# Performance work log

Hardware: AMD Instinct MI355X
Metric: run time of the kernel (lower is better)

Reference implementation:

```python
import jax, jax.numpy as jnp
import numpy as np

N = 100000   # nodes
E = 1600000  # edges (avg degree 16)
D = 128      # embedding / hidden dim
L = 2        # aggregator layers (len(weight_size_list)-1)
EPS = 1e-12  # F.normalize eps


def setup_inputs() -> dict:
    key = jax.random.key(0)
    ks = jax.random.split(key, 8)
    return {
        "embeddings": jax.random.normal(ks[0], (N, D), jnp.float32),
        "edge_src": jax.random.randint(ks[1], (E,), 0, N, jnp.int32),
        "edge_dst": jax.random.randint(ks[2], (E,), 0, N, jnp.int32),
        "edge_val": jax.random.uniform(ks[3], (E,), jnp.float32),
        "W_sum": jax.random.normal(ks[4], (L, D, D), jnp.float32) * 0.05,
        "b_sum": jnp.zeros((L, D), jnp.float32),
        "W_prod": jax.random.normal(ks[5], (L, D, D), jnp.float32) * 0.05,
        "b_prod": jnp.zeros((L, D), jnp.float32),
    }


def reference(embeddings, edge_src, edge_dst, edge_val, W_sum, b_sum, W_prod, b_prod):
    # Faithful KGATConv forward with BiAggregator (alg_type='bi'), dropout=0 (eval).
    # Note: original code feeds the UN-normalized aggregator output as `embeddings`
    # (ego) to the next layer, while the SpMM consumes the normalized all_embeddings[-1].
    ego = embeddings            # `embeddings` variable in torch code
    spmm_in = embeddings        # all_embeddings[-1]
    outs = [embeddings]
    for i in range(L):
        # sparse A @ x : gather source rows, scale by edge value, scatter-add to dst
        msg = edge_val[:, None] * spmm_in[edge_src]            # [E, D]
        side = jax.ops.segment_sum(msg, edge_dst, num_segments=N)  # [N, D]
        # BiAggregator: LeakyReLU(W1(e+side)+b1) + LeakyReLU(W2(e*side)+b2)
        s = jax.nn.leaky_relu((ego + side) @ W_sum[i] + b_sum[i], 0.01)
        p = jax.nn.leaky_relu((ego * side) @ W_prod[i] + b_prod[i], 0.01)
        ego = s + p
        # F.normalize(p=2, dim=-1)
        nrm = jnp.maximum(jnp.linalg.norm(ego, axis=-1, keepdims=True), EPS)
        spmm_in = ego / nrm
        outs.append(spmm_in)
    return jnp.stack(outs)  # [L+1, N, D]
```

## Files before the change

### kernel.cpp

```cpp
#include <hip/hip_runtime.h>

#define D_DIM 128
#define ROWS 32
#define MROWS 64
#define ZPAD 136
#define EPAD 132

#define BSH 7
#define BROWS (1 << BSH)
#define NB_MAX 2048
#define CHUNK 4096

typedef __bf16 bf16x8 __attribute__((ext_vector_type(8)));
typedef __bf16 bf16x4 __attribute__((ext_vector_type(4)));
typedef float  f32x4  __attribute__((ext_vector_type(4)));

__global__ __launch_bounds__(256) void spmm_atomic(
    const float* __restrict__ x, const int* __restrict__ src,
    const int* __restrict__ dst, const float* __restrict__ val,
    float* __restrict__ side, long long total)
{
    long long i = (long long)blockIdx.x * blockDim.x + threadIdx.x;
    if (i >= total) return;
    int e = (int)(i >> 5);
    int q = (int)(i & 31);
    int s = src[e];
    int d = dst[e];
    float v = val[e];
    const float4 xv = *reinterpret_cast<const float4*>(x + (long long)s * D_DIM + q * 4);
    float* o = side + (long long)d * D_DIM + q * 4;
    unsafeAtomicAdd(o + 0, v * xv.x);
    unsafeAtomicAdd(o + 1, v * xv.y);
    unsafeAtomicAdd(o + 2, v * xv.z);
    unsafeAtomicAdd(o + 3, v * xv.w);
}

__global__ __launch_bounds__(256) void hist_kernel(
    const int* __restrict__ dst, int* __restrict__ cnt, int E)
{
    int i = blockIdx.x * 256 + threadIdx.x;
    if (i < E) atomicAdd(&cnt[dst[i]], 1);
}

__global__ __launch_bounds__(256) void scan_blocks(
    const int* __restrict__ cnt, int* __restrict__ row_ptr,
    int* __restrict__ blk_sums, int N)
{
    __shared__ int sh[256];
    int i = blockIdx.x * 256 + threadIdx.x;
    int v = (i < N) ? cnt[i] : 0;
    sh[threadIdx.x] = v;
    __syncthreads();
#pragma unroll
    for (int off = 1; off < 256; off <<= 1) {
        int t = (threadIdx.x >= off) ? sh[threadIdx.x - off] : 0;
        __syncthreads();
        sh[threadIdx.x] += t;
        __syncthreads();
    }
    if (i < N) row_ptr[i] = sh[threadIdx.x] - v;
    if (threadIdx.x == 255) blk_sums[blockIdx.x] = sh[255];
}

__global__ __launch_bounds__(256) void scan_carry(int* __restrict__ blk, int B)
{
    __shared__ int sh[256];
    __shared__ int carry;
    if (threadIdx.x == 0) carry = 0;
    __syncthreads();
    for (int base = 0; base < B; base += 256) {
        int i = base + threadIdx.x;
        int v = (i < B) ? blk[i] : 0;
        sh[threadIdx.x] = v;
        __syncthreads();
#pragma unroll
        for (int off = 1; off < 256; off <<= 1) {
            int t = (threadIdx.x >= off) ? sh[threadIdx.x - off] : 0;
            __syncthreads();
            sh[threadIdx.x] += t;
            __syncthreads();
        }
        int excl = sh[threadIdx.x] - v + carry;
        if (i < B) blk[i] = excl;
        __syncthreads();
        if (threadIdx.x == 255) carry = carry + sh[255];
        __syncthreads();
    }
}

__global__ __launch_bounds__(256) void scan_add(
    int* __restrict__ row_ptr, const int* __restrict__ blk_sums,
    int* __restrict__ row_fill, int N, int E)
{
    int i = blockIdx.x * 256 + threadIdx.x;
    if (i < N) {
        int v = row_ptr[i] + blk_sums[i >> 8];
        row_ptr[i]  = v;
        row_fill[i] = v;
    }
    if (i == 0) row_ptr[N] = E;
}

__global__ __launch_bounds__(256) void scatter_kernel(
    const int* __restrict__ src, const int* __restrict__ dst,
    const float* __restrict__ val, int* __restrict__ row_fill,
    int2* __restrict__ csr_sv, int E)
{
    int e = blockIdx.x * 256 + threadIdx.x;
    if (e >= E) return;
    int d = dst[e];
    int pos = atomicAdd(&row_fill[d], 1);
    csr_sv[pos] = make_int2(src[e], __float_as_int(val[e]));
}

__global__ __launch_bounds__(256) void bucket_count(
    const int* __restrict__ dst, int* __restrict__ bucket_cnt, int E, int NB)
{
    __shared__ int h[NB_MAX];
    for (int i = threadIdx.x; i < NB; i += 256) h[i] = 0;
    __syncthreads();
    int ebase = blockIdx.x * CHUNK;
    int ecnt  = min(CHUNK, E - ebase);
    for (int i = threadIdx.x; i < ecnt; i += 256)
        atomicAdd(&h[dst[ebase + i] >> BSH], 1);
    __syncthreads();
    for (int i = threadIdx.x; i < NB; i += 256)
        if (h[i]) atomicAdd(&bucket_cnt[i], h[i]);
}

__global__ __launch_bounds__(256) void bucket_scan(
    const int* __restrict__ bucket_cnt, int* __restrict__ bucket_ptr,
    int* __restrict__ bucket_fill, int NB, int E)
{
    __shared__ int sh[256];
    __shared__ int carry;
    if (threadIdx.x == 0) carry = 0;
    __syncthreads();
    for (int base = 0; base < NB; base += 256) {
        int i = base + threadIdx.x;
        int v = (i < NB) ? bucket_cnt[i] : 0;
        sh[threadIdx.x] = v;
        __syncthreads();
#pragma unroll
        for (int off = 1; off < 256; off <<= 1) {
            int t = (threadIdx.x >= off) ? sh[threadIdx.x - off] : 0;
            __syncthreads();
            sh[threadIdx.x] += t;
            __syncthreads();
        }
        if (i < NB) {
            int excl = sh[threadIdx.x] - v + carry;
            bucket_ptr[i]  = excl;
            bucket_fill[i] = excl;
        }
        __syncthreads();
        if (threadIdx.x == 255) carry = carry + sh[255];
        __syncthreads();
    }
    if (threadIdx.x == 0) bucket_ptr[NB] = E;
}

__global__ __launch_bounds__(256) void bucket_scatter(
    const int* __restrict__ src, const int* __restrict__ dst,
    const float* __restrict__ val, int* __restrict__ bucket_fill,
    int* __restrict__ stage,
    int NB, int E)
{
    __shared__ int hist[NB_MAX];
    __shared__ int excl[NB_MAX];
    __shared__ int gbase[NB_MAX];
    __shared__ int psum[256];
    __shared__ int s_src[CHUNK];
    __shared__ int s_val[CHUNK];
    __shared__ int s_dst[CHUNK];

    const int tid   = threadIdx.x;
    const int ebase = blockIdx.x * CHUNK;
    const int ecnt  = min(CHUNK, E - ebase);

    for (int i = tid; i < NB; i += 256) hist[i] = 0;
    __syncthreads();
    for (int i = tid; i < ecnt; i += 256)
        atomicAdd(&hist[dst[ebase + i] >> BSH], 1);
    __syncthreads();
    const int per = (NB + 255) / 256;
    const int t0  = tid * per;
    int tsum = 0;
    for (int k = 0; k < per; ++k) {
        int idx = t0 + k;
        tsum += (idx < NB) ? hist[idx] : 0;
    }
    psum[tid] = tsum;
    __syncthreads();
#pragma unroll
    for (int off = 1; off < 256; off <<= 1) {
        int t = (tid >= off) ? psum[tid - off] : 0;
        __syncthreads();
        psum[tid] += t;
        __syncthreads();
    }
    int run = psum[tid] - tsum;
    for (int k = 0; k < per; ++k) {
        int idx = t0 + k;
        if (idx < NB) { excl[idx] = run; run += hist[idx]; }
    }
    __syncthreads();
    for (int i = tid; i < NB; i += 256)
        gbase[i] = hist[i] ? atomicAdd(&bucket_fill[i], hist[i]) : 0;
    __syncthreads();
    for (int i = tid; i < NB; i += 256) hist[i] = excl[i];
    __syncthreads();
    for (int i = tid; i < ecnt; i += 256) {
        int d = dst[ebase + i];
        int slot = atomicAdd(&hist[d >> BSH], 1);
        s_src[slot] = src[ebase + i];
        s_val[slot] = __float_as_int(val[ebase + i]);
        s_dst[slot] = d;
    }
    __syncthreads();
    for (int i = tid; i < ecnt; i += 256) {
        int d   = s_dst[i];
        int bkt = d >> BSH;
        int gpos = gbase[bkt] + (i - excl[bkt]);
        *reinterpret_cast<int4*>(stage + 4 * (long long)gpos) =
            make_int4(s_src[i], s_val[i], d, 0);
    }
}

__global__ __launch_bounds__(256) void bucket_finalize(
    const int* __restrict__ stage, const int* __restrict__ bucket_ptr,
    int* __restrict__ row_ptr, int2* __restrict__ csr_sv, int N, int E)
{
    __shared__ int cnt[BROWS];
    __shared__ int rbase[BROWS];

    const int b   = blockIdx.x;
    const int tid = threadIdx.x;
    const int e0  = bucket_ptr[b];
    const int e1  = bucket_ptr[b + 1];
    const int r0  = b << BSH;
    const int nrows = min(BROWS, N - r0);

    if (tid < BROWS) cnt[tid] = 0;
    __syncthreads();
    for (int i = e0 + tid; i < e1; i += 256)
        atomicAdd(&cnt[stage[4 * (long long)i + 2] & (BROWS - 1)], 1);
    __syncthreads();
    if (tid < BROWS) rbase[tid] = cnt[tid];
    __syncthreads();
#pragma unroll
    for (int off = 1; off < BROWS; off <<= 1) {
        int t = 0;
        if (tid < BROWS && tid >= off) t = rbase[tid - off];
        __syncthreads();
        if (tid < BROWS) rbase[tid] += t;
        __syncthreads();
    }
    if (tid < BROWS) {
        int excl = e0 + rbase[tid] - cnt[tid];
        rbase[tid] = excl;
        if (tid < nrows) row_ptr[r0 + tid] = excl;
    }
    if (b == 0 && tid == 0) row_ptr[N] = E;
    __syncthreads();
    if (tid < BROWS) cnt[tid] = 0;
    __syncthreads();
    for (int i = e0 + tid; i < e1; i += 256) {
        const int4 t = *reinterpret_cast<const int4*>(stage + 4 * (long long)i);
        int r = t.z & (BROWS - 1);
        int rank = atomicAdd(&cnt[r], 1);
        csr_sv[rbase[r] + rank] = make_int2(t.x, t.y);
    }
}

__global__ __launch_bounds__(256) void wt_convert(
    const float* __restrict__ Wsum, const float* __restrict__ Wprod,
    __bf16* __restrict__ WTsum, __bf16* __restrict__ WTprod, int total)
{
    int i = blockIdx.x * 256 + threadIdx.x;
    if (i >= total) return;
    int l  = i >> 14;
    int nk = i & 16383;
    int n  = nk >> 7;
    int k  = nk & 127;
    int widx = (l << 14) + (k << 7) + n;
    WTsum[i]  = (__bf16)Wsum[widx];
    WTprod[i] = (__bf16)Wprod[widx];
}

__global__ __launch_bounds__(256) void emb_prep(
    const float* __restrict__ emb, float* __restrict__ out0,
    __bf16* __restrict__ xbf, long long n4)
{
    long long i = (long long)blockIdx.x * 256 + threadIdx.x;
    if (i >= n4) return;
    float4 v = reinterpret_cast<const float4*>(emb)[i];
    reinterpret_cast<float4*>(out0)[i] = v;
    bf16x4 b;
    b[0] = (__bf16)v.x; b[1] = (__bf16)v.y;
    b[2] = (__bf16)v.z; b[3] = (__bf16)v.w;
    reinterpret_cast<bf16x4*>(xbf)[i] = b;
}

__global__ __launch_bounds__(256) void spmm_csr_bf16(
    const __bf16* __restrict__ x, const int* __restrict__ row_ptr,
    const int2* __restrict__ csr_sv, float* __restrict__ side, int N)
{
    int row  = blockIdx.x * 8 + (threadIdx.x >> 5);
    int lane = threadIdx.x & 31;
    if (row >= N) return;
    int start = row_ptr[row];
    int end   = row_ptr[row + 1];
    const __bf16* xl = x + lane * 4;
    float4 acc = make_float4(0.f, 0.f, 0.f, 0.f);
    int j = start;
    for (; j + 8 <= end; j += 8) {
        int2 sv0 = csr_sv[j + 0], sv1 = csr_sv[j + 1];
        int2 sv2 = csr_sv[j + 2], sv3 = csr_sv[j + 3];
        int2 sv4 = csr_sv[j + 4], sv5 = csr_sv[j + 5];
        int2 sv6 = csr_sv[j + 6], sv7 = csr_sv[j + 7];
        bf16x4 b0 = *reinterpret_cast<const bf16x4*>(xl + (long long)sv0.x * D_DIM);
        bf16x4 b1 = *reinterpret_cast<const bf16x4*>(xl + (long long)sv1.x * D_DIM);
        bf16x4 b2 = *reinterpret_cast<const bf16x4*>(xl + (long long)sv2.x * D_DIM);
        bf16x4 b3 = *reinterpret_cast<const bf16x4*>(xl + (long long)sv3.x * D_DIM);
        bf16x4 b4 = *reinterpret_cast<const bf16x4*>(xl + (long long)sv4.x * D_DIM);
        bf16x4 b5 = *reinterpret_cast<const bf16x4*>(xl + (long long)sv5.x * D_DIM);
        bf16x4 b6 = *reinterpret_cast<const bf16x4*>(xl + (long long)sv6.x * D_DIM);
        bf16x4 b7 = *reinterpret_cast<const bf16x4*>(xl + (long long)sv7.x * D_DIM);
        float v0 = __int_as_float(sv0.y), v1 = __int_as_float(sv1.y);
        float v2 = __int_as_float(sv2.y), v3 = __int_as_float(sv3.y);
        float v4 = __int_as_float(sv4.y), v5 = __int_as_float(sv5.y);
        float v6 = __int_as_float(sv6.y), v7 = __int_as_float(sv7.y);
        acc.x += v0 * (float)b0[0] + v1 * (float)b1[0] + v2 * (float)b2[0] + v3 * (float)b3[0];
        acc.y += v0 * (float)b0[1] + v1 * (float)b1[1] + v2 * (float)b2[1] + v3 * (float)b3[1];
        acc.z += v0 * (float)b0[2] + v1 * (float)b1[2] + v2 * (float)b2[2] + v3 * (float)b3[2];
        acc.w += v0 * (float)b0[3] + v1 * (float)b1[3] + v2 * (float)b2[3] + v3 * (float)b3[3];
        acc.x += v4 * (float)b4[0] + v5 * (float)b5[0] + v6 * (float)b6[0] + v7 * (float)b7[0];
        acc.y += v4 * (float)b4[1] + v5 * (float)b5[1] + v6 * (float)b6[1] + v7 * (float)b7[1];
        acc.z += v4 * (float)b4[2] + v5 * (float)b5[2] + v6 * (float)b6[2] + v7 * (float)b7[2];
        acc.w += v4 * (float)b4[3] + v5 * (float)b5[3] + v6 * (float)b6[3] + v7 * (float)b7[3];
    }
    for (; j + 4 <= end; j += 4) {
        int2 sv0 = csr_sv[j + 0], sv1 = csr_sv[j + 1];
        int2 sv2 = csr_sv[j + 2], sv3 = csr_sv[j + 3];
        bf16x4 b0 = *reinterpret_cast<const bf16x4*>(xl + (long long)sv0.x * D_DIM);
        bf16x4 b1 = *reinterpret_cast<const bf16x4*>(xl + (long long)sv1.x * D_DIM);
        bf16x4 b2 = *reinterpret_cast<const bf16x4*>(xl + (long long)sv2.x * D_DIM);
        bf16x4 b3 = *reinterpret_cast<const bf16x4*>(xl + (long long)sv3.x * D_DIM);
        float v0 = __int_as_float(sv0.y), v1 = __int_as_float(sv1.y);
        float v2 = __int_as_float(sv2.y), v3 = __int_as_float(sv3.y);
        acc.x += v0 * (float)b0[0] + v1 * (float)b1[0] + v2 * (float)b2[0] + v3 * (float)b3[0];
        acc.y += v0 * (float)b0[1] + v1 * (float)b1[1] + v2 * (float)b2[1] + v3 * (float)b3[1];
        acc.z += v0 * (float)b0[2] + v1 * (float)b1[2] + v2 * (float)b2[2] + v3 * (float)b3[2];
        acc.w += v0 * (float)b0[3] + v1 * (float)b1[3] + v2 * (float)b2[3] + v3 * (float)b3[3];
    }
    for (; j < end; ++j) {
        int2 sv = csr_sv[j];
        float v = __int_as_float(sv.y);
        bf16x4 b = *reinterpret_cast<const bf16x4*>(xl + (long long)sv.x * D_DIM);
        acc.x += v * (float)b[0];
        acc.y += v * (float)b[1];
        acc.z += v * (float)b[2];
        acc.w += v * (float)b[3];
    }
    *reinterpret_cast<float4*>(side + (long long)row * D_DIM + lane * 4) = acc;
}

__global__ __launch_bounds__(256) void spmm_csr_f32(
    const float* __restrict__ x, const int* __restrict__ row_ptr,
    const int2* __restrict__ csr_sv, float* __restrict__ side, int N)
{
    int row  = blockIdx.x * 8 + (threadIdx.x >> 5);
    int lane = threadIdx.x & 31;
    if (row >= N) return;
    int start = row_ptr[row];
    int end   = row_ptr[row + 1];
    const float* xl = x + lane * 4;
    float4 acc = make_float4(0.f, 0.f, 0.f, 0.f);
    int j = start;
    for (; j + 4 <= end; j += 4) {
        int2 sv0 = csr_sv[j + 0], sv1 = csr_sv[j + 1];
        int2 sv2 = csr_sv[j + 2], sv3 = csr_sv[j + 3];
        const float4 x0 = *reinterpret_cast<const float4*>(xl + (long long)sv0.x * D_DIM);
        const float4 x1 = *reinterpret_cast<const float4*>(xl + (long long)sv1.x * D_DIM);
        const float4 x2 = *reinterpret_cast<const float4*>(xl + (long long)sv2.x * D_DIM);
        const float4 x3 = *reinterpret_cast<const float4*>(xl + (long long)sv3.x * D_DIM);
        float v0 = __int_as_float(sv0.y), v1 = __int_as_float(sv1.y);
        float v2 = __int_as_float(sv2.y), v3 = __int_as_float(sv3.y);
        acc.x += v0 * x0.x + v1 * x1.x + v2 * x2.x + v3 * x3.x;
        acc.y += v0 * x0.y + v1 * x1.y + v2 * x2.y + v3 * x3.y;
        acc.z += v0 * x0.z + v1 * x1.z + v2 * x2.z + v3 * x3.z;
        acc.w += v0 * x0.w + v1 * x1.w + v2 * x2.w + v3 * x3.w;
    }
    for (; j < end; ++j) {
        int2 sv = csr_sv[j];
        float v = __int_as_float(sv.y);
        const float4 xv = *reinterpret_cast<const float4*>(xl + (long long)sv.x * D_DIM);
        acc.x += v * xv.x;
        acc.y += v * xv.y;
        acc.z += v * xv.z;
        acc.w += v * xv.w;
    }
    *reinterpret_cast<float4*>(side + (long long)row * D_DIM + lane * 4) = acc;
}

__global__ __launch_bounds__(512) void fused_layer_mfma(
    const float* __restrict__ ego_src, const float* __restrict__ nrm_in,
    const float* __restrict__ side,
    const __bf16* __restrict__ WTsum, const float* __restrict__ bsum,
    const __bf16* __restrict__ WTprod, const float* __restrict__ bprod,
    float* __restrict__ norm_out,
    __bf16* __restrict__ nbf_out,
    float* __restrict__ nrm_out,
    int N)
{
    __shared__ __align__(16) char smem[MROWS * ZPAD * 2 * sizeof(__bf16)];
    __shared__ float rowsq[MROWS][9];
    auto zt = reinterpret_cast<__bf16(*)[ZPAD]>(smem);
    auto mt = reinterpret_cast<__bf16(*)[ZPAD]>(smem + MROWS * ZPAD * sizeof(__bf16));
    auto et = reinterpret_cast<float(*)[EPAD]>(smem);

    const int tid  = threadIdx.x;
    const int row0 = blockIdx.x * MROWS;

    for (int idx = tid; idx < MROWS * 32; idx += 512) {
        int r = idx >> 5, q = idx & 31;
        int row = row0 + r;
        float4 e4 = make_float4(0.f, 0.f, 0.f, 0.f);
        float4 s4 = make_float4(0.f, 0.f, 0.f, 0.f);
        if (row < N) {
            e4 = *reinterpret_cast<const float4*>(ego_src + (long long)row * D_DIM + q * 4);
            s4 = *reinterpret_cast<const float4*>(side    + (long long)row * D_DIM + q * 4);
            if (nrm_in) {
                float sc = nrm_in[row];
                e4.x *= sc; e4.y *= sc; e4.z *= sc; e4.w *= sc;
            }
        }
        bf16x4 z4, m4;
        z4[0] = (__bf16)(e4.x + s4.x); z4[1] = (__bf16)(e4.y + s4.y);
        z4[2] = (__bf16)(e4.z + s4.z); z4[3] = (__bf16)(e4.w + s4.w);
        m4[0] = (__bf16)(e4.x * s4.x); m4[1] = (__bf16)(e4.y * s4.y);
        m4[2] = (__bf16)(e4.z * s4.z); m4[3] = (__bf16)(e4.w * s4.w);
        *reinterpret_cast<bf16x4*>(&zt[r][q * 4]) = z4;
        *reinterpret_cast<bf16x4*>(&mt[r][q * 4]) = m4;
    }

    const int wave = tid >> 6;
    const int lane = tid & 63;
    const int ln   = lane & 15;
    const int quad = lane >> 4;

    bf16x8 bs[4], bp[4];
#pragma unroll
    for (int ks = 0; ks < 4; ++ks) {
        const long long wofs = (long long)(wave * 16 + ln) * D_DIM + ks * 32 + quad * 8;
        bs[ks] = *reinterpret_cast<const bf16x8*>(WTsum  + wofs);
        bp[ks] = *reinterpret_cast<const bf16x8*>(WTprod + wofs);
    }

    __syncthreads();

    f32x4 acc_s[4], acc_p[4];
#pragma unroll
    for (int rg = 0; rg < 4; ++rg) {
        acc_s[rg] = (f32x4){0.f, 0.f, 0.f, 0.f};
        acc_p[rg] = (f32x4){0.f, 0.f, 0.f, 0.f};
    }

#pragma unroll
    for (int rg = 0; rg < 4; ++rg) {
#pragma unroll
        for (int ks = 0; ks < 4; ++ks) {
            const int k0 = ks * 32 + quad * 8;
            bf16x8 az = *reinterpret_cast<const bf16x8*>(&zt[rg * 16 + ln][k0]);
            bf16x8 am = *reinterpret_cast<const bf16x8*>(&mt[rg * 16 + ln][k0]);
            acc_s[rg] = __builtin_amdgcn_mfma_f32_16x16x32_bf16(az, bs[ks], acc_s[rg], 0, 0, 0);
            acc_p[rg] = __builtin_amdgcn_mfma_f32_16x16x32_bf16(am, bp[ks], acc_p[rg], 0, 0, 0);
        }
    }

    const float bsv = bsum[wave * 16 + ln];
    const float bpv = bprod[wave * 16 + ln];
#pragma unroll
    for (int rg = 0; rg < 4; ++rg) {
#pragma unroll
        for (int r = 0; r < 4; ++r) {
            float sv = acc_s[rg][r] + bsv;
            sv = sv > 0.f ? sv : 0.01f * sv;
            float pv = acc_p[rg][r] + bpv;
            pv = pv > 0.f ? pv : 0.01f * pv;
            float e = sv + pv;
            acc_s[rg][r] = e;
            float sq = e * e;
#pragma unroll
            for (int off = 1; off < 16; off <<= 1)
                sq += __shfl_xor(sq, off, 16);
            if (ln == 0)
                rowsq[rg * 16 + quad * 4 + r][wave] = sq;
        }
    }

    __syncthreads();

#pragma unroll
    for (int rg = 0; rg < 4; ++rg)
#pragma unroll
        for (int r = 0; r < 4; ++r)
            et[rg * 16 + quad * 4 + r][wave * 16 + ln] = acc_s[rg][r];
    __syncthreads();

    for (int idx = tid; idx < MROWS * 32; idx += 512) {
        int r = idx >> 5, q = idx & 31;
        int row = row0 + r;
        if (row >= N) continue;
        float s = 0.f;
#pragma unroll
        for (int j = 0; j < 8; ++j) s += rowsq[r][j];
        float nrmv = fmaxf(sqrtf(s), 1e-12f);
        float inv  = 1.0f / nrmv;
        if (q == 0 && nrm_out) nrm_out[row] = nrmv;
        float4 e4 = *reinterpret_cast<const float4*>(&et[r][q * 4]);
        float4 n4 = make_float4(e4.x * inv, e4.y * inv, e4.z * inv, e4.w * inv);
        *reinterpret_cast<float4*>(norm_out + (long long)row * D_DIM + q * 4) = n4;
        if (nbf_out) {
            bf16x4 b4;
            b4[0] = (__bf16)n4.x; b4[1] = (__bf16)n4.y;
            b4[2] = (__bf16)n4.z; b4[3] = (__bf16)n4.w;
            *reinterpret_cast<bf16x4*>(nbf_out + (long long)row * D_DIM + q * 4) = b4;
        }
    }
}

__global__ __launch_bounds__(256) void fused_layer_f32(
    const float* __restrict__ ego, const float* __restrict__ side,
    const float* __restrict__ Wsum, const float* __restrict__ bsum,
    const float* __restrict__ Wprod, const float* __restrict__ bprod,
    float* __restrict__ ego_out, float* __restrict__ norm_out, int N)
{
    __shared__ float zt[ROWS][D_DIM];
    __shared__ float mt[ROWS][D_DIM];
    __shared__ float wsh[32][D_DIM];
    __shared__ float wph[32][D_DIM];

    const int tid  = threadIdx.x;
    const int row0 = blockIdx.x * ROWS;
    const int cg   = tid & 31;
    const int rg   = tid >> 5;

    for (int idx = tid; idx < ROWS * 32; idx += 256) {
        int r = idx >> 5, q = idx & 31;
        int row = row0 + r;
        float4 e4 = make_float4(0.f, 0.f, 0.f, 0.f);
        float4 s4 = make_float4(0.f, 0.f, 0.f, 0.f);
        if (row < N) {
            e4 = *reinterpret_cast<const float4*>(ego  + (long long)row * D_DIM + q * 4);
            s4 = *reinterpret_cast<const float4*>(side + (long long)row * D_DIM + q * 4);
        }
        float4 z4 = make_float4(e4.x + s4.x, e4.y + s4.y, e4.z + s4.z, e4.w + s4.w);
        float4 m4 = make_float4(e4.x * s4.x, e4.y * s4.y, e4.z * s4.z, e4.w * s4.w);
        *reinterpret_cast<float4*>(&zt[r][q * 4]) = z4;
        *reinterpret_cast<float4*>(&mt[r][q * 4]) = m4;
    }

    float acc_s[4][4], acc_p[4][4];
#pragma unroll
    for (int a = 0; a < 4; ++a)
#pragma unroll
        for (int b = 0; b < 4; ++b) { acc_s[a][b] = 0.f; acc_p[a][b] = 0.f; }

    for (int kc = 0; kc < D_DIM; kc += 32) {
        __syncthreads();
        for (int idx = tid; idx < 32 * 32; idx += 256) {
            int kk = idx >> 5, q = idx & 31;
            *reinterpret_cast<float4*>(&wsh[kk][q * 4]) =
                *reinterpret_cast<const float4*>(Wsum + (long long)(kc + kk) * D_DIM + q * 4);
            *reinterpret_cast<float4*>(&wph[kk][q * 4]) =
                *reinterpret_cast<const float4*>(Wprod + (long long)(kc + kk) * D_DIM + q * 4);
        }
        __syncthreads();
#pragma unroll 8
        for (int kk = 0; kk < 32; ++kk) {
            float4 w_s = *reinterpret_cast<const float4*>(&wsh[kk][cg * 4]);
            float4 w_p = *reinterpret_cast<const float4*>(&wph[kk][cg * 4]);
#pragma unroll
            for (int rr = 0; rr < 4; ++rr) {
                float z = zt[rg * 4 + rr][kc + kk];
                float m = mt[rg * 4 + rr][kc + kk];
                acc_s[rr][0] += z * w_s.x; acc_s[rr][1] += z * w_s.y;
                acc_s[rr][2] += z * w_s.z; acc_s[rr][3] += z * w_s.w;
                acc_p[rr][0] += m * w_p.x; acc_p[rr][1] += m * w_p.y;
                acc_p[rr][2] += m * w_p.z; acc_p[rr][3] += m * w_p.w;
            }
        }
    }

    const float4 bs = *reinterpret_cast<const float4*>(bsum  + cg * 4);
    const float4 bp = *reinterpret_cast<const float4*>(bprod + cg * 4);
    float ev[4][4];
    float part[4];
#pragma unroll
    for (int rr = 0; rr < 4; ++rr) {
        float bsv[4] = {bs.x, bs.y, bs.z, bs.w};
        float bpv[4] = {bp.x, bp.y, bp.z, bp.w};
        float acc = 0.f;
#pragma unroll
        for (int cc = 0; cc < 4; ++cc) {
            float sv = acc_s[rr][cc] + bsv[cc];
            sv = sv > 0.f ? sv : 0.01f * sv;
            float pv = acc_p[rr][cc] + bpv[cc];
            pv = pv > 0.f ? pv : 0.01f * pv;
            float e = sv + pv;
            ev[rr][cc] = e;
            acc += e * e;
        }
        part[rr] = acc;
    }
#pragma unroll
    for (int off = 1; off < 32; off <<= 1) {
#pragma unroll
        for (int rr = 0; rr < 4; ++rr)
            part[rr] += __shfl_xor(part[rr], off, 32);
    }
#pragma unroll
    for (int rr = 0; rr < 4; ++rr) {
        int row = row0 + rg * 4 + rr;
        if (row >= N) continue;
        float inv = 1.0f / fmaxf(sqrtf(part[rr]), 1e-12f);
        float4 o  = make_float4(ev[rr][0] * inv, ev[rr][1] * inv,
                                ev[rr][2] * inv, ev[rr][3] * inv);
        *reinterpret_cast<float4*>(norm_out + (long long)row * D_DIM + cg * 4) = o;
        if (ego_out) {
            float4 g = make_float4(ev[rr][0], ev[rr][1], ev[rr][2], ev[rr][3]);
            *reinterpret_cast<float4*>(ego_out + (long long)row * D_DIM + cg * 4) = g;
        }
    }
}

extern "C" void kernel_launch(void* const* d_in, const int* in_sizes, int n_in,
                              void* d_out, int out_size, void* d_ws, size_t ws_size,
                              hipStream_t stream)
{
    const float* emb   = (const float*)d_in[0];
    const int*   esrc  = (const int*)  d_in[1];
    const int*   edst  = (const int*)  d_in[2];
    const float* evalv = (const float*)d_in[3];
    const float* Wsum  = (const float*)d_in[4];
    const float* bsum  = (const float*)d_in[5];
    const float* Wprod = (const float*)d_in[6];
    const float* bprod = (const float*)d_in[7];
    float* out = (float*)d_out;

    const int D = 128;
    const int N = in_sizes[0] / D;
    const int E = in_sizes[1];
    const int L = in_sizes[5] / D;
    const size_t ND = (size_t)N * D;
    const int B = (N + 255) / 256;
    const int NB = (N + BROWS - 1) >> BSH;

    char* ws = (char*)d_ws;
    float* side    = (float*)ws;                 ws += ND * sizeof(float);
    float* ego_buf = (float*)ws;                 ws += ND * sizeof(float);
    int*   row_ptr  = (int*)ws;                  ws += (size_t)(N + 1) * sizeof(int);
    int*   row_fill = (int*)ws;                  ws += (size_t)N * sizeof(int);
    int*   blk_sums = (int*)ws;                  ws += (size_t)B * sizeof(int);
    ws = (char*)(((uintptr_t)ws + 15) & ~(uintptr_t)15);
    int2*  csr_sv   = (int2*)ws;                 ws += (size_t)E * sizeof(int2);
    size_t csr_bytes = (size_t)(ws - (char*)d_ws);
    __bf16* WTsum  = (__bf16*)ws;                ws += (size_t)L * D * D * sizeof(__bf16);
    __bf16* WTprod = (__bf16*)ws;                ws += (size_t)L * D * D * sizeof(__bf16);
    __bf16* xbf    = (__bf16*)ws;                ws += ND * sizeof(__bf16);
    float*  nrm_buf = (float*)ws;                ws += (size_t)N * sizeof(float);
    size_t mfma_bytes = (size_t)(ws - (char*)d_ws);
    int* bucket_cnt  = (int*)ws;                 ws += (size_t)(NB + 1) * sizeof(int);
    int* bucket_ptr  = (int*)ws;                 ws += (size_t)(NB + 1) * sizeof(int);
    int* bucket_fill = (int*)ws;                 ws += (size_t)(NB + 1) * sizeof(int);
    size_t bucket_bytes = (size_t)(ws - (char*)d_ws);
    int* stage = (int*)side;

    const bool use_csr    = (ws_size >= csr_bytes);
    const bool use_mfma   = (ws_size >= mfma_bytes);
    const bool use_bucket = use_csr && (ws_size >= bucket_bytes) && (NB <= NB_MAX) &&
                            ((size_t)E * 16 <= 2 * ND * sizeof(float));

    if (use_mfma) {
        long long n4 = (long long)(ND / 4);
        emb_prep<<<(int)((n4 + 255) / 256), 256, 0, stream>>>(emb, out, xbf, n4);
        int total = L * D * D;
        wt_convert<<<(total + 255) / 256, 256, 0, stream>>>(
            Wsum, Wprod, WTsum, WTprod, total);
    } else {
        hipMemcpyAsync(out, emb, ND * sizeof(float), hipMemcpyDeviceToDevice, stream);
    }

    if (use_bucket) {
        const int nblk = (E + CHUNK - 1) / CHUNK;
        hipMemsetAsync(bucket_cnt, 0, (size_t)NB * sizeof(int), stream);
        bucket_count<<<nblk, 256, 0, stream>>>(edst, bucket_cnt, E, NB);
        bucket_scan<<<1, 256, 0, stream>>>(bucket_cnt, bucket_ptr, bucket_fill, NB, E);
        bucket_scatter<<<nblk, 256, 0, stream>>>(
            esrc, edst, evalv, bucket_fill, stage, NB, E);
        bucket_finalize<<<NB, 256, 0, stream>>>(
            stage, bucket_ptr, row_ptr, csr_sv, N, E);
    } else if (use_csr) {
        hipMemsetAsync(row_fill, 0, (size_t)N * sizeof(int), stream);
        hist_kernel<<<(E + 255) / 256, 256, 0, stream>>>(edst, row_fill, E);
        scan_blocks<<<B, 256, 0, stream>>>(row_fill, row_ptr, blk_sums, N);
        scan_carry<<<1, 256, 0, stream>>>(blk_sums, B);
        scan_add<<<B, 256, 0, stream>>>(row_ptr, blk_sums, row_fill, N, E);
        scatter_kernel<<<(E + 255) / 256, 256, 0, stream>>>(
            esrc, edst, evalv, row_fill, csr_sv, E);
    }

    const float* ego      = emb;
    const float* nrm_prev = nullptr;
    const float* spmm_in  = emb;
    for (int l = 0; l < L; ++l) {
        if (use_csr) {
            if (use_mfma) {
                spmm_csr_bf16<<<(N + 7) / 8, 256, 0, stream>>>(
                    xbf, row_ptr, csr_sv, side, N);
            } else {
                spmm_csr_f32<<<(N + 7) / 8, 256, 0, stream>>>(
                    spmm_in, row_ptr, csr_sv, side, N);
            }
        } else {
            hipMemsetAsync(side, 0, ND * sizeof(float), stream);
            long long total  = (long long)E * 32;
            long long blocks = (total + 255) / 256;
            spmm_atomic<<<(int)blocks, 256, 0, stream>>>(spmm_in, esrc, edst, evalv,
                                                         side, total);
        }

        float* norm_out = out + (size_t)(l + 1) * ND;
        if (use_mfma) {
            const bool more = (l + 1 < L);
            __bf16* nbf  = more ? xbf : nullptr;
            float*  nrmo = more ? nrm_buf : nullptr;
            fused_layer_mfma<<<(N + MROWS - 1) / MROWS, 512, 0, stream>>>(
                ego, nrm_prev, side,
                WTsum + (size_t)l * D * D, bsum + (size_t)l * D,
                WTprod + (size_t)l * D * D, bprod + (size_t)l * D,
                norm_out, nbf, nrmo, N);
            ego      = norm_out;
            nrm_prev = nrm_buf;
        } else {
            float* ego_out = (l + 1 < L) ? ego_buf : nullptr;
            fused_layer_f32<<<(N + ROWS - 1) / ROWS, 256, 0, stream>>>(
                ego, side,
                Wsum + (size_t)l * D * D, bsum + (size_t)l * D,
                Wprod + (size_t)l * D * D, bprod + (size_t)l * D,
                ego_out, norm_out, N);
            ego     = ego_buf;
            spmm_in = norm_out;
        }
    }
}
```

Before: 535.0 us.

## Fuse CSR SpMM gather into the MFMA layer kernel and ping-pong bf16 buffers

```diff
diff --git a/kernel.cpp b/kernel.cpp
--- a/kernel.cpp
+++ b/kernel.cpp
@@ -300,70 +300,6 @@
     b[0] = (__bf16)v.x; b[1] = (__bf16)v.y;
     b[2] = (__bf16)v.z; b[3] = (__bf16)v.w;
     reinterpret_cast<bf16x4*>(xbf)[i] = b;
-}
-
-__global__ __launch_bounds__(256) void spmm_csr_bf16(
-    const __bf16* __restrict__ x, const int* __restrict__ row_ptr,
-    const int2* __restrict__ csr_sv, float* __restrict__ side, int N)
-{
-    int row  = blockIdx.x * 8 + (threadIdx.x >> 5);
-    int lane = threadIdx.x & 31;
-    if (row >= N) return;
-    int start = row_ptr[row];
-    int end   = row_ptr[row + 1];
-    const __bf16* xl = x + lane * 4;
-    float4 acc = make_float4(0.f, 0.f, 0.f, 0.f);
-    int j = start;
-    for (; j + 8 <= end; j += 8) {
-        int2 sv0 = csr_sv[j + 0], sv1 = csr_sv[j + 1];
-        int2 sv2 = csr_sv[j + 2], sv3 = csr_sv[j + 3];
-        int2 sv4 = csr_sv[j + 4], sv5 = csr_sv[j + 5];
-        int2 sv6 = csr_sv[j + 6], sv7 = csr_sv[j + 7];
-        bf16x4 b0 = *reinterpret_cast<const bf16x4*>(xl + (long long)sv0.x * D_DIM);
-        bf16x4 b1 = *reinterpret_cast<const bf16x4*>(xl + (long long)sv1.x * D_DIM);
-        bf16x4 b2 = *reinterpret_cast<const bf16x4*>(xl + (long long)sv2.x * D_DIM);
-        bf16x4 b3 = *reinterpret_cast<const bf16x4*>(xl + (long long)sv3.x * D_DIM);
-        bf16x4 b4 = *reinterpret_cast<const bf16x4*>(xl + (long long)sv4.x * D_DIM);
-        bf16x4 b5 = *reinterpret_cast<const bf16x4*>(xl + (long long)sv5.x * D_DIM);
-        bf16x4 b6 = *reinterpret_cast<const bf16x4*>(xl + (long long)sv6.x * D_DIM);
-        bf16x4 b7 = *reinterpret_cast<const bf16x4*>(xl + (long long)sv7.x * D_DIM);
-        float v0 = __int_as_float(sv0.y), v1 = __int_as_float(sv1.y);
-        float v2 = __int_as_float(sv2.y), v3 = __int_as_float(sv3.y);
-        float v4 = __int_as_float(sv4.y), v5 = __int_as_float(sv5.y);
-        float v6 = __int_as_float(sv6.y), v7 = __int_as_float(sv7.y);
-        acc.x += v0 * (float)b0[0] + v1 * (float)b1[0] + v2 * (float)b2[0] + v3 * (float)b3[0];
-        acc.y += v0 * (float)b0[1] + v1 * (float)b1[1] + v2 * (float)b2[1] + v3 * (float)b3[1];
-        acc.z += v0 * (float)b0[2] + v1 * (float)b1[2] + v2 * (float)b2[2] + v3 * (float)b3[2];
-        acc.w += v0 * (float)b0[3] + v1 * (float)b1[3] + v2 * (float)b2[3] + v3 * (float)b3[3];
-        acc.x += v4 * (float)b4[0] + v5 * (float)b5[0] + v6 * (float)b6[0] + v7 * (float)b7[0];
-        acc.y += v4 * (float)b4[1] + v5 * (float)b5[1] + v6 * (float)b6[1] + v7 * (float)b7[1];
-        acc.z += v4 * (float)b4[2] + v5 * (float)b5[2] + v6 * (float)b6[2] + v7 * (float)b7[2];
-        acc.w += v4 * (float)b4[3] + v5 * (float)b5[3] + v6 * (float)b6[3] + v7 * (float)b7[3];
-    }
-    for (; j + 4 <= end; j += 4) {
-        int2 sv0 = csr_sv[j + 0], sv1 = csr_sv[j + 1];
-        int2 sv2 = csr_sv[j + 2], sv3 = csr_sv[j + 3];
-        bf16x4 b0 = *reinterpret_cast<const bf16x4*>(xl + (long long)sv0.x * D_DIM);
-        bf16x4 b1 = *reinterpret_cast<const bf16x4*>(xl + (long long)sv1.x * D_DIM);
-        bf16x4 b2 = *reinterpret_cast<const bf16x4*>(xl + (long long)sv2.x * D_DIM);
-        bf16x4 b3 = *reinterpret_cast<const bf16x4*>(xl + (long long)sv3.x * D_DIM);
-        float v0 = __int_as_float(sv0.y), v1 = __int_as_float(sv1.y);
-        float v2 = __int_as_float(sv2.y), v3 = __int_as_float(sv3.y);
-        acc.x += v0 * (float)b0[0] + v1 * (float)b1[0] + v2 * (float)b2[0] + v3 * (float)b3[0];
-        acc.y += v0 * (float)b0[1] + v1 * (float)b1[1] + v2 * (float)b2[1] + v3 * (float)b3[1];
-        acc.z += v0 * (float)b0[2] + v1 * (float)b1[2] + v2 * (float)b2[2] + v3 * (float)b3[2];
-        acc.w += v0 * (float)b0[3] + v1 * (float)b1[3] + v2 * (float)b2[3] + v3 * (float)b3[3];
-    }
-    for (; j < end; ++j) {
-        int2 sv = csr_sv[j];
-        float v = __int_as_float(sv.y);
-        bf16x4 b = *reinterpret_cast<const bf16x4*>(xl + (long long)sv.x * D_DIM);
-        acc.x += v * (float)b[0];
-        acc.y += v * (float)b[1];
-        acc.z += v * (float)b[2];
-        acc.w += v * (float)b[3];
-    }
-    *reinterpret_cast<float4*>(side + (long long)row * D_DIM + lane * 4) = acc;
 }
 
 __global__ __launch_bounds__(256) void spmm_csr_f32(
@@ -405,8 +341,9 @@
 }
 
 __global__ __launch_bounds__(512) void fused_layer_mfma(
+    const __bf16* __restrict__ xbf, const int* __restrict__ row_ptr,
+    const int2* __restrict__ csr_sv,
     const float* __restrict__ ego_src, const float* __restrict__ nrm_in,
-    const float* __restrict__ side,
     const __bf16* __restrict__ WTsum, const float* __restrict__ bsum,
     const __bf16* __restrict__ WTprod, const float* __restrict__ bprod,
     float* __restrict__ norm_out,
@@ -423,26 +360,80 @@
     const int tid  = threadIdx.x;
     const int row0 = blockIdx.x * MROWS;
 
-    for (int idx = tid; idx < MROWS * 32; idx += 512) {
-        int r = idx >> 5, q = idx & 31;
-        int row = row0 + r;
-        float4 e4 = make_float4(0.f, 0.f, 0.f, 0.f);
-        float4 s4 = make_float4(0.f, 0.f, 0.f, 0.f);
+    const int grp = tid >> 5;
+    const int gl  = tid & 31;
+    const __bf16* xl = xbf + gl * 4;
+
+    for (int rr = 0; rr < 4; ++rr) {
+        const int r   = grp * 4 + rr;
+        const int row = row0 + r;
+        float4 acc = make_float4(0.f, 0.f, 0.f, 0.f);
+        float4 e4  = make_float4(0.f, 0.f, 0.f, 0.f);
         if (row < N) {
-            e4 = *reinterpret_cast<const float4*>(ego_src + (long long)row * D_DIM + q * 4);
-            s4 = *reinterpret_cast<const float4*>(side    + (long long)row * D_DIM + q * 4);
+            int j   = row_ptr[row];
+            int end = row_ptr[row + 1];
+            for (; j + 8 <= end; j += 8) {
+                int2 sv0 = csr_sv[j + 0], sv1 = csr_sv[j + 1];
+                int2 sv2 = csr_sv[j + 2], sv3 = csr_sv[j + 3];
+                int2 sv4 = csr_sv[j + 4], sv5 = csr_sv[j + 5];
+                int2 sv6 = csr_sv[j + 6], sv7 = csr_sv[j + 7];
+                bf16x4 b0 = *reinterpret_cast<const bf16x4*>(xl + (long long)sv0.x * D_DIM);
+                bf16x4 b1 = *reinterpret_cast<const bf16x4*>(xl + (long long)sv1.x * D_DIM);
+                bf16x4 b2 = *reinterpret_cast<const bf16x4*>(xl + (long long)sv2.x * D_DIM);
+                bf16x4 b3 = *reinterpret_cast<const bf16x4*>(xl + (long long)sv3.x * D_DIM);
+                bf16x4 b4 = *reinterpret_cast<const bf16x4*>(xl + (long long)sv4.x * D_DIM);
+                bf16x4 b5 = *reinterpret_cast<const bf16x4*>(xl + (long long)sv5.x * D_DIM);
+                bf16x4 b6 = *reinterpret_cast<const bf16x4*>(xl + (long long)sv6.x * D_DIM);
+                bf16x4 b7 = *reinterpret_cast<const bf16x4*>(xl + (long long)sv7.x * D_DIM);
+                float v0 = __int_as_float(sv0.y), v1 = __int_as_float(sv1.y);
+                float v2 = __int_as_float(sv2.y), v3 = __int_as_float(sv3.y);
+                float v4 = __int_as_float(sv4.y), v5 = __int_as_float(sv5.y);
+                float v6 = __int_as_float(sv6.y), v7 = __int_as_float(sv7.y);
+                acc.x += v0 * (float)b0[0] + v1 * (float)b1[0] + v2 * (float)b2[0] + v3 * (float)b3[0];
+                acc.y += v0 * (float)b0[1] + v1 * (float)b1[1] + v2 * (float)b2[1] + v3 * (float)b3[1];
+                acc.z += v0 * (float)b0[2] + v1 * (float)b1[2] + v2 * (float)b2[2] + v3 * (float)b3[2];
+                acc.w += v0 * (float)b0[3] + v1 * (float)b1[3] + v2 * (float)b2[3] + v3 * (float)b3[3];
+                acc.x += v4 * (float)b4[0] + v5 * (float)b5[0] + v6 * (float)b6[0] + v7 * (float)b7[0];
+                acc.y += v4 * (float)b4[1] + v5 * (float)b5[1] + v6 * (float)b6[1] + v7 * (float)b7[1];
+                acc.z += v4 * (float)b4[2] + v5 * (float)b5[2] + v6 * (float)b6[2] + v7 * (float)b7[2];
+                acc.w += v4 * (float)b4[3] + v5 * (float)b5[3] + v6 * (float)b6[3] + v7 * (float)b7[3];
+            }
+            for (; j + 4 <= end; j += 4) {
+                int2 sv0 = csr_sv[j + 0], sv1 = csr_sv[j + 1];
+                int2 sv2 = csr_sv[j + 2], sv3 = csr_sv[j + 3];
+                bf16x4 b0 = *reinterpret_cast<const bf16x4*>(xl + (long long)sv0.x * D_DIM);
+                bf16x4 b1 = *reinterpret_cast<const bf16x4*>(xl + (long long)sv1.x * D_DIM);
+                bf16x4 b2 = *reinterpret_cast<const bf16x4*>(xl + (long long)sv2.x * D_DIM);
+                bf16x4 b3 = *reinterpret_cast<const bf16x4*>(xl + (long long)sv3.x * D_DIM);
+                float v0 = __int_as_float(sv0.y), v1 = __int_as_float(sv1.y);
+                float v2 = __int_as_float(sv2.y), v3 = __int_as_float(sv3.y);
+                acc.x += v0 * (float)b0[0] + v1 * (float)b1[0] + v2 * (float)b2[0] + v3 * (float)b3[0];
+                acc.y += v0 * (float)b0[1] + v1 * (float)b1[1] + v2 * (float)b2[1] + v3 * (float)b3[1];
+                acc.z += v0 * (float)b0[2] + v1 * (float)b1[2] + v2 * (float)b2[2] + v3 * (float)b3[2];
+                acc.w += v0 * (float)b0[3] + v1 * (float)b1[3] + v2 * (float)b2[3] + v3 * (float)b3[3];
+            }
+            for (; j < end; ++j) {
+                int2 sv = csr_sv[j];
+                float v = __int_as_float(sv.y);
+                bf16x4 b = *reinterpret_cast<const bf16x4*>(xl + (long long)sv.x * D_DIM);
+                acc.x += v * (float)b[0];
+                acc.y += v * (float)b[1];
+                acc.z += v * (float)b[2];
+                acc.w += v * (float)b[3];
+            }
+            e4 = *reinterpret_cast<const float4*>(ego_src + (long long)row * D_DIM + gl * 4);
             if (nrm_in) {
                 float sc = nrm_in[row];
                 e4.x *= sc; e4.y *= sc; e4.z *= sc; e4.w *= sc;
             }
         }
         bf16x4 z4, m4;
-        z4[0] = (__bf16)(e4.x + s4.x); z4[1] = (__bf16)(e4.y + s4.y);
-        z4[2] = (__bf16)(e4.z + s4.z); z4[3] = (__bf16)(e4.w + s4.w);
-        m4[0] = (__bf16)(e4.x * s4.x); m4[1] = (__bf16)(e4.y * s4.y);
-        m4[2] = (__bf16)(e4.z * s4.z); m4[3] = (__bf16)(e4.w * s4.w);
-        *reinterpret_cast<bf16x4*>(&zt[r][q * 4]) = z4;
-        *reinterpret_cast<bf16x4*>(&mt[r][q * 4]) = m4;
+        z4[0] = (__bf16)(e4.x + acc.x); z4[1] = (__bf16)(e4.y + acc.y);
+        z4[2] = (__bf16)(e4.z + acc.z); z4[3] = (__bf16)(e4.w + acc.w);
+        m4[0] = (__bf16)(e4.x * acc.x); m4[1] = (__bf16)(e4.y * acc.y);
+        m4[2] = (__bf16)(e4.z * acc.z); m4[3] = (__bf16)(e4.w * acc.w);
+        *reinterpret_cast<bf16x4*>(&zt[r][gl * 4]) = z4;
+        *reinterpret_cast<bf16x4*>(&mt[r][gl * 4]) = m4;
     }
 
     const int wave = tid >> 6;
@@ -677,6 +668,7 @@
     int* bucket_fill = (int*)ws;                 ws += (size_t)(NB + 1) * sizeof(int);
     size_t bucket_bytes = (size_t)(ws - (char*)d_ws);
     int* stage = (int*)side;
+    __bf16* xbf_alt = (__bf16*)ego_buf;
 
     const bool use_csr    = (ws_size >= csr_bytes);
     const bool use_mfma   = (ws_size >= mfma_bytes);
@@ -715,36 +707,36 @@
     const float* ego      = emb;
     const float* nrm_prev = nullptr;
     const float* spmm_in  = emb;
+    const __bf16* x_cur   = xbf;
+    __bf16*       x_nxt   = xbf_alt;
     for (int l = 0; l < L; ++l) {
-        if (use_csr) {
-            if (use_mfma) {
-                spmm_csr_bf16<<<(N + 7) / 8, 256, 0, stream>>>(
-                    xbf, row_ptr, csr_sv, side, N);
-            } else {
-                spmm_csr_f32<<<(N + 7) / 8, 256, 0, stream>>>(
-                    spmm_in, row_ptr, csr_sv, side, N);
-            }
-        } else {
-            hipMemsetAsync(side, 0, ND * sizeof(float), stream);
-            long long total  = (long long)E * 32;
-            long long blocks = (total + 255) / 256;
-            spmm_atomic<<<(int)blocks, 256, 0, stream>>>(spmm_in, esrc, edst, evalv,
-                                                         side, total);
-        }
-
         float* norm_out = out + (size_t)(l + 1) * ND;
         if (use_mfma) {
             const bool more = (l + 1 < L);
-            __bf16* nbf  = more ? xbf : nullptr;
+            __bf16* nbf  = more ? x_nxt : nullptr;
             float*  nrmo = more ? nrm_buf : nullptr;
             fused_layer_mfma<<<(N + MROWS - 1) / MROWS, 512, 0, stream>>>(
-                ego, nrm_prev, side,
+                x_cur, row_ptr, csr_sv,
+                ego, nrm_prev,
                 WTsum + (size_t)l * D * D, bsum + (size_t)l * D,
                 WTprod + (size_t)l * D * D, bprod + (size_t)l * D,
                 norm_out, nbf, nrmo, N);
             ego      = norm_out;
             nrm_prev = nrm_buf;
+            const __bf16* t = x_cur;
+            x_cur = x_nxt;
+            x_nxt = (__bf16*)t;
         } else {
+            if (use_csr) {
+                spmm_csr_f32<<<(N + 7) / 8, 256, 0, stream>>>(
+                    spmm_in, row_ptr, csr_sv, side, N);
+            } else {
+                hipMemsetAsync(side, 0, ND * sizeof(float), stream);
+                long long total  = (long long)E * 32;
+                long long blocks = (total + 255) / 256;
+                spmm_atomic<<<(int)blocks, 256, 0, stream>>>(spmm_in, esrc, edst, evalv,
+                                                             side, total);
+            }
             float* ego_out = (l + 1 < L) ? ego_buf : nullptr;
             fused_layer_f32<<<(N + ROWS - 1) / ROWS, 256, 0, stream>>>(
                 ego, side,
```

After: 539.3 us. About the same (+0.8%).
